# Kernel optimization log

Hardware: AMD Instinct MI355X
Metric: run time of the kernel (lower is better)

The kernel has to match this reference:

```python
import jax, jax.numpy as jnp
import numpy as np

HIDDEN = 512
HEADS = 8
HEAD_DIM = HIDDEN // HEADS


def setup_inputs() -> dict:
    key = jax.random.key(0)
    ks = jax.random.split(key, 12)
    B, N, C = 4, 2048, HIDDEN
    s = 1.0 / np.sqrt(C)
    inp = {
        "query_content": jax.random.normal(ks[0], (B, N, C), dtype=jnp.float32),
        "query_pos": jax.random.uniform(ks[1], (B, N, 4), dtype=jnp.float32),
        "Wq": jax.random.uniform(ks[2], (C, C), jnp.float32, -s, s),
        "bq": jax.random.uniform(ks[3], (C,), jnp.float32, -s, s),
        "Wk": jax.random.uniform(ks[4], (C, C), jnp.float32, -s, s),
        "bk": jax.random.uniform(ks[5], (C,), jnp.float32, -s, s),
        "Wv": jax.random.uniform(ks[6], (C, C), jnp.float32, -s, s),
        "bv": jax.random.uniform(ks[7], (C,), jnp.float32, -s, s),
        "Wo": jax.random.uniform(ks[8], (C, C), jnp.float32, -s, s),
        "bo": jax.random.uniform(ks[9], (C,), jnp.float32, -s, s),
        "gamma": jnp.ones((C,), jnp.float32),
        "beta": jnp.zeros((C,), jnp.float32),
    }
    return inp


def _iof_bias(query_pos):
    # query_pos: [B, N, 4] -> bias [B, N, N] = -0.1 * sqrt(dx^2 + dy^2 + eps)
    x = query_pos[..., 0]
    y = query_pos[..., 1]
    dx = jnp.abs(x[:, :, None] - x[:, None, :])
    dy = jnp.abs(y[:, :, None] - y[:, None, :])
    dist = jnp.sqrt(dx * dx + dy * dy + 1e-8)
    return -0.1 * dist


def reference(query_content, query_pos, Wq, bq, Wk, bk, Wv, bv, Wo, bo, gamma, beta):
    B, N, C = query_content.shape
    H, D = HEADS, HEAD_DIM
    # torch Linear: x @ W.T + b
    Q = (query_content @ Wq.T + bq).reshape(B, N, H, D).transpose(0, 2, 1, 3)
    K = (query_content @ Wk.T + bk).reshape(B, N, H, D).transpose(0, 2, 1, 3)
    V = (query_content @ Wv.T + bv).reshape(B, N, H, D).transpose(0, 2, 1, 3)
    scores = jnp.einsum("bhnd,bhmd->bhnm", Q, K) / jnp.sqrt(jnp.float32(D))
    scores = scores + _iof_bias(query_pos)[:, None, :, :]
    attn = jax.nn.softmax(scores, axis=-1)
    out = jnp.einsum("bhnm,bhmd->bhnd", attn, V)
    out = out.transpose(0, 2, 1, 3).reshape(B, N, C)
    out = out @ Wo.T + bo
    h = out + query_content
    mu = jnp.mean(h, axis=-1, keepdims=True)
    var = jnp.var(h, axis=-1, keepdims=True)
    return (h - mu) / jnp.sqrt(var + 1e-5) * gamma + beta
```

## Files before the change

kernel.cpp:

```cpp
#include <hip/hip_runtime.h>
#include <hip/hip_bf16.h>

#define C_DIM 512
#define H_NUM 8
#define D_DIM 64
#define B_NUM 4
#define N_SEQ 2048
#define M_TOT (B_NUM*N_SEQ)

typedef unsigned short u16;
typedef unsigned int   u32;
typedef __attribute__((ext_vector_type(8))) short short8;
typedef __attribute__((ext_vector_type(4))) float f32x4;

#define MFMA16 __builtin_amdgcn_mfma_f32_16x16x32_bf16

__device__ __forceinline__ u16 f2b(float f) {
    union { float f; u32 u; } v; v.f = f;
    u32 r = v.u + 0x7FFFu + ((v.u >> 16) & 1u);
    return (u16)(r >> 16);
}
__device__ __forceinline__ float fexp2(float x) {
    float r;
    asm("v_exp_f32 %0, %1" : "=v"(r) : "v"(x));
    return r;
}
__device__ __forceinline__ float b2f_lo(u32 u) {
    union { u32 u; float f; } v; v.u = u << 16; return v.f;
}
__device__ __forceinline__ float b2f_hi(u32 u) {
    union { u32 u; float f; } v; v.u = u & 0xFFFF0000u; return v.f;
}
__device__ __forceinline__ void gload16(const u16* g, u16* l) {
    __builtin_amdgcn_global_load_lds(
        (const __attribute__((address_space(1))) void*)g,
        (__attribute__((address_space(3))) void*)l, 16, 0, 0);
}
__device__ __forceinline__ void cast8(const float* s, u16* d) {
    const float4* p = (const float4*)s;
    float4 a = p[0], b = p[1];
    short8 v;
    v[0] = (short)f2b(a.x); v[1] = (short)f2b(a.y);
    v[2] = (short)f2b(a.z); v[3] = (short)f2b(a.w);
    v[4] = (short)f2b(b.x); v[5] = (short)f2b(b.y);
    v[6] = (short)f2b(b.z); v[7] = (short)f2b(b.w);
    *(short8*)d = v;
}

__global__ __launch_bounds__(256) void k_prep(const float* __restrict__ qc,
                                              const float* __restrict__ Wq,
                                              const float* __restrict__ Wk,
                                              const float* __restrict__ Wv,
                                              const float* __restrict__ Wo,
                                              const float* __restrict__ bq,
                                              const float* __restrict__ bk,
                                              const float* __restrict__ bv,
                                              const float* __restrict__ bo,
                                              const float* __restrict__ qpos,
                                              u16* __restrict__ xb,
                                              u16* __restrict__ wb,
                                              float* __restrict__ bqkv,
                                              u16* __restrict__ bias)
{
    const int bid = blockIdx.x, t = threadIdx.x;
    if (bid < 2048) {
        int i = bid * 256 + t;
        cast8(qc + (size_t)i * 8, xb + (size_t)i * 8);
    } else if (bid < 2560) {
        int r = bid - 2048;
        int y = r >> 7;
        const float* s = (y == 0) ? Wq : (y == 1) ? Wk : (y == 2) ? Wv : Wo;
        int i = (r & 127) * 256 + t;
        cast8(s + (size_t)i * 8, wb + (size_t)y * 262144 + (size_t)i * 8);
    } else if (bid < 2568) {
        int idx = (bid - 2560) * 256 + t;
        float v = idx < 512 ? bq[idx] : idx < 1024 ? bk[idx - 512]
                : idx < 1536 ? bv[idx - 1024] : bo[idx - 1536];
        bqkv[idx] = v;
    } else {
        int r = bid - 2568;
        int i = r & 2047, b = r >> 11;
        const float4 qi = *(const float4*)(qpos + (size_t)(b * 2048 + i) * 4);
        const float4* pj = (const float4*)(qpos + ((size_t)b * 2048 + t * 8) * 4);
        const float NC = -0.1f * 1.4426950408889634f;
        short8 v;
        #pragma unroll
        for (int jj = 0; jj < 8; ++jj) {
            float4 pk = pj[jj];
            float dx = qi.x - pk.x, dy = qi.y - pk.y;
            float d2 = fmaf(dx, dx, fmaf(dy, dy, 1e-8f));
            v[jj] = (short)f2b(sqrtf(d2) * NC);
        }
        *(short8*)(bias + (size_t)(b * 2048 + i) * 2048 + t * 8) = v;
    }
}

__global__ __launch_bounds__(256) void k_gemm(const u16* __restrict__ A,
                                              const u16* __restrict__ Bw,
                                              const float* __restrict__ bias,
                                              const float* __restrict__ qc,
                                              u16* __restrict__ oq,
                                              u16* __restrict__ ok,
                                              u16* __restrict__ ov,
                                              float* __restrict__ outf,
                                              int fixed_mode)
{
    __shared__ alignas(16) u16 la[3][4][128][8];
    __shared__ alignas(16) u16 lb[3][4][128][8];
    const int t = threadIdx.x;
    const int nwg = gridDim.x * gridDim.y;
    const int wgid = blockIdx.y * gridDim.x + blockIdx.x;
    const int swz = (wgid & 7) * (nwg >> 3) + (wgid >> 3);
    const int ntn = gridDim.y;
    const int m0 = (swz / ntn) * 128, n0 = (swz % ntn) * 128;
    const int w = t >> 6, l = t & 63, lr = l & 15, kg = l >> 4;
    const int wm = w >> 1, wn = w & 1;
    const int NS = C_DIM / 32;

    f32x4 acc[4][4] = {};

    const int srow = t & 127;
    const u16* As0 = A + (size_t)(m0 + srow) * C_DIM + (t >> 7) * 8;
    const u16* Bs0 = Bw + (size_t)(n0 + srow) * C_DIM + (t >> 7) * 8;

    #pragma unroll
    for (int s = 0; s < 2; ++s) {
        u16* ldA = (u16*)la[s] + w * 512;
        u16* ldB = (u16*)lb[s] + w * 512;
        gload16(As0 + s * 32,      ldA);
        gload16(As0 + s * 32 + 16, ldA + 2048);
        gload16(Bs0 + s * 32,      ldB);
        gload16(Bs0 + s * 32 + 16, ldB + 2048);
    }
    asm volatile("s_waitcnt vmcnt(4)" ::: "memory");
    __builtin_amdgcn_s_barrier();

    for (int s = 0; s < NS; ++s) {
        const int bi = s % 3;
        if (s + 2 < NS) {
            const int bn = (s + 2) % 3;
            u16* ldA = (u16*)la[bn] + w * 512;
            u16* ldB = (u16*)lb[bn] + w * 512;
            gload16(As0 + (s + 2) * 32,      ldA);
            gload16(As0 + (s + 2) * 32 + 16, ldA + 2048);
            gload16(Bs0 + (s + 2) * 32,      ldB);
            gload16(Bs0 + (s + 2) * 32 + 16, ldB + 2048);
        }
        __builtin_amdgcn_sched_barrier(0);

        short8 af[4], bf[4];
        #pragma unroll
        for (int fm = 0; fm < 4; ++fm)
            af[fm] = *(const short8*)la[bi][kg][wm * 64 + fm * 16 + lr];
        #pragma unroll
        for (int fn = 0; fn < 4; ++fn)
            bf[fn] = *(const short8*)lb[bi][kg][wn * 64 + fn * 16 + lr];
        __builtin_amdgcn_s_setprio(1);
        #pragma unroll
        for (int fm = 0; fm < 4; ++fm)
        #pragma unroll
        for (int fn = 0; fn < 4; ++fn)
            acc[fm][fn] = MFMA16(af[fm], bf[fn], acc[fm][fn], 0, 0, 0);
        __builtin_amdgcn_s_setprio(0);

        if (s + 1 < NS) {
            if (s + 2 < NS) asm volatile("s_waitcnt vmcnt(4)" ::: "memory");
            else            asm volatile("s_waitcnt vmcnt(0)" ::: "memory");
            __builtin_amdgcn_s_barrier();
        }
    }

    const int mode = (fixed_mode == 3) ? 3 : (n0 >> 9);

    if (mode == 3) {
        #pragma unroll
        for (int fm = 0; fm < 4; ++fm)
        #pragma unroll
        for (int fn = 0; fn < 4; ++fn) {
            int c = n0 + wn * 64 + fn * 16 + lr;
            float bv_ = bias[c];
            #pragma unroll
            for (int i = 0; i < 4; ++i) {
                int m = m0 + wm * 64 + fm * 16 + kg * 4 + i;
                outf[(size_t)m * C_DIM + c] = acc[fm][fn][i] + bv_ + qc[(size_t)m * C_DIM + c];
            }
        }
    } else if (mode == 2) {
        #pragma unroll
        for (int fm = 0; fm < 4; ++fm)
        #pragma unroll
        for (int fn = 0; fn < 4; ++fn) {
            int c = n0 + wn * 64 + fn * 16 + lr;
            int cc = c & 511, h = cc >> 6, d = cc & 63;
            float bv_ = bias[c];
            int m = m0 + wm * 64 + fm * 16 + kg * 4;
            int bb = m >> 11, n = m & 2047;
            uint2 pk;
            pk.x = ((u32)f2b(acc[fm][fn][1] + bv_) << 16) | f2b(acc[fm][fn][0] + bv_);
            pk.y = ((u32)f2b(acc[fm][fn][3] + bv_) << 16) | f2b(acc[fm][fn][2] + bv_);
            *(uint2*)(ov + ((size_t)(bb * H_NUM + h) * D_DIM + d) * N_SEQ + n) = pk;
        }
    } else {
        u16* outb = (mode == 0) ? oq : ok;
        #pragma unroll
        for (int fm = 0; fm < 4; ++fm)
        #pragma unroll
        for (int fn = 0; fn < 4; ++fn) {
            int c = n0 + wn * 64 + fn * 16 + lr;
            int cc = c & 511, h = cc >> 6, d = cc & 63;
            float bv_ = bias[c];
            #pragma unroll
            for (int i = 0; i < 4; ++i) {
                int m = m0 + wm * 64 + fm * 16 + kg * 4 + i;
                int bb = m >> 11, n = m & 2047;
                outb[((size_t)(bb * H_NUM + h) * N_SEQ + n) * D_DIM + d] = f2b(bv_ + acc[fm][fn][i]);
            }
        }
    }
}

__global__ __launch_bounds__(512, 4) void k_flash(const u16* __restrict__ Q,
                                                  const u16* __restrict__ K,
                                                  const u16* __restrict__ Vt,
                                                  const u16* __restrict__ bias,
                                                  u16* __restrict__ attn_out)
{
    __shared__ alignas(16) u16 kbuf[3][64][64];
    __shared__ alignas(16) u16 vbuf[3][64][64];
    __shared__ alignas(16) u16 pbuf[8][16][64];

    const int t = threadIdx.x;
    const int w = t >> 6, l = t & 63, lr = l & 15, g = l >> 4;
    const int flat = blockIdx.y * 16 + blockIdx.x;
    const int h = flat >> 6, b = (flat >> 4) & 3, qt = flat & 15;
    const int bh = b * H_NUM + h;
    const int q = qt * 128 + w * 16 + lr;
    const int sx = lr & 7;

    const float SC = 0.125f * 1.4426950408889634f;
    const int NT = N_SEQ / 64;

    const u16* Qb = Q + ((size_t)bh * N_SEQ + q) * D_DIM;
    const u16* Kb = K + (size_t)bh * N_SEQ * D_DIM;
    const u16* Vb = Vt + (size_t)bh * D_DIM * N_SEQ;
    const u16* Bb = bias + ((size_t)b * N_SEQ + q) * N_SEQ;

    short8 aq0 = *(const short8*)(Qb + g * 8);
    short8 aq1 = *(const short8*)(Qb + 32 + g * 8);

    const int sr = t >> 3;
    const int ssl = (t & 7) ^ (sr & 7);
    const u16* gK = Kb + (size_t)sr * D_DIM + ssl * 8;
    const u16* gV = Vb + (size_t)sr * N_SEQ + ssl * 8;

    f32x4 acc[4] = {};
    float lac0 = 0.f, lac1 = 0.f, lac2 = 0.f, lac3 = 0.f;
    uint2 bcur[4], bnxt[4];

    gload16(gK,              (u16*)&kbuf[0][0][0] + w * 512);
    gload16(gV,              (u16*)&vbuf[0][0][0] + w * 512);
    gload16(gK + 64 * D_DIM, (u16*)&kbuf[1][0][0] + w * 512);
    gload16(gV + 64,         (u16*)&vbuf[1][0][0] + w * 512);
    __builtin_amdgcn_sched_barrier(0);
    #pragma unroll
    for (int fn = 0; fn < 4; ++fn)
        bcur[fn] = *(const uint2*)(Bb + fn * 16 + g * 4);
    __builtin_amdgcn_sched_barrier(0);
    asm volatile("s_waitcnt vmcnt(6)" ::: "memory");
    __builtin_amdgcn_s_barrier();

    for (int kt = 0; kt < NT; ++kt) {
        const int bi = kt % 3;
        if (kt + 1 < NT) {
            #pragma unroll
            for (int fn = 0; fn < 4; ++fn)
                bnxt[fn] = *(const uint2*)(Bb + (kt + 1) * 64 + fn * 16 + g * 4);
        }
        __builtin_amdgcn_sched_barrier(0);
        if (kt + 2 < NT) {
            const int bn = (kt + 2) % 3;
            gload16(gK + (size_t)(kt + 2) * 64 * D_DIM, (u16*)&kbuf[bn][0][0] + w * 512);
            gload16(gV + (kt + 2) * 64,                 (u16*)&vbuf[bn][0][0] + w * 512);
        }
        __builtin_amdgcn_sched_barrier(0);

        f32x4 st[4] = {};
        __builtin_amdgcn_s_setprio(1);
        #pragma unroll
        for (int fn = 0; fn < 4; ++fn) {
            short8 ak0 = *(const short8*)&kbuf[bi][fn * 16 + lr][(g ^ sx) * 8];
            short8 ak1 = *(const short8*)&kbuf[bi][fn * 16 + lr][((4 + g) ^ sx) * 8];
            st[fn] = MFMA16(ak0, aq0, st[fn], 0, 0, 0);
            st[fn] = MFMA16(ak1, aq1, st[fn], 0, 0, 0);
        }
        __builtin_amdgcn_s_setprio(0);

        float sv[16];
        #pragma unroll
        for (int fn = 0; fn < 4; ++fn) {
            sv[fn * 4 + 0] = fmaf(st[fn][0], SC, b2f_lo(bcur[fn].x));
            sv[fn * 4 + 1] = fmaf(st[fn][1], SC, b2f_hi(bcur[fn].x));
            sv[fn * 4 + 2] = fmaf(st[fn][2], SC, b2f_lo(bcur[fn].y));
            sv[fn * 4 + 3] = fmaf(st[fn][3], SC, b2f_hi(bcur[fn].y));
        }
        #pragma unroll
        for (int j = 0; j < 4; ++j)  { sv[j]  = fexp2(sv[j]);  lac0 += sv[j]; }
        #pragma unroll
        for (int j = 4; j < 8; ++j)  { sv[j]  = fexp2(sv[j]);  lac1 += sv[j]; }
        #pragma unroll
        for (int j = 8; j < 12; ++j) { sv[j]  = fexp2(sv[j]);  lac2 += sv[j]; }
        #pragma unroll
        for (int j = 12; j < 16; ++j){ sv[j]  = fexp2(sv[j]);  lac3 += sv[j]; }

        #pragma unroll
        for (int fn = 0; fn < 4; ++fn) {
            union { float f; u32 u; } p0, p1, p2, p3;
            p0.f = sv[fn * 4 + 0]; p1.f = sv[fn * 4 + 1];
            p2.f = sv[fn * 4 + 2]; p3.f = sv[fn * 4 + 3];
            uint2 pk;
            pk.x = (p1.u & 0xFFFF0000u) | (p0.u >> 16);
            pk.y = (p3.u & 0xFFFF0000u) | (p2.u >> 16);
            int slot = fn * 2 + (g >> 1);
            *(uint2*)&pbuf[w][lr][(slot ^ sx) * 8 + (g & 1) * 4] = pk;
        }
        asm volatile("s_waitcnt lgkmcnt(0)" ::: "memory");
        __builtin_amdgcn_sched_barrier(0);

        short8 bp0 = *(const short8*)&pbuf[w][lr][(g ^ sx) * 8];
        short8 bp1 = *(const short8*)&pbuf[w][lr][((4 + g) ^ sx) * 8];

        __builtin_amdgcn_s_setprio(1);
        #pragma unroll
        for (int df = 0; df < 4; ++df) {
            short8 av0 = *(const short8*)&vbuf[bi][df * 16 + lr][(g ^ sx) * 8];
            short8 av1 = *(const short8*)&vbuf[bi][df * 16 + lr][((4 + g) ^ sx) * 8];
            acc[df] = MFMA16(av0, bp0, acc[df], 0, 0, 0);
            acc[df] = MFMA16(av1, bp1, acc[df], 0, 0, 0);
        }
        __builtin_amdgcn_s_setprio(0);

        #pragma unroll
        for (int fn = 0; fn < 4; ++fn) bcur[fn] = bnxt[fn];

        if (kt + 1 < NT) {
            if (kt + 2 < NT) asm volatile("s_waitcnt vmcnt(6)" ::: "memory");
            else             asm volatile("s_waitcnt vmcnt(4)" ::: "memory");
            __builtin_amdgcn_s_barrier();
        }
    }

    float l_run = (lac0 + lac1) + (lac2 + lac3);
    l_run += __shfl_xor(l_run, 16);
    l_run += __shfl_xor(l_run, 32);
    float rl;
    asm("v_rcp_f32 %0, %1" : "=v"(rl) : "v"(l_run));
    rl = rl * (2.f - l_run * rl);
    u16* ob = attn_out + ((size_t)(b * N_SEQ + q)) * C_DIM + h * D_DIM + g * 4;
    #pragma unroll
    for (int df = 0; df < 4; ++df) {
        u32 w0 = ((u32)f2b(acc[df][1] * rl) << 16) | f2b(acc[df][0] * rl);
        u32 w1 = ((u32)f2b(acc[df][3] * rl) << 16) | f2b(acc[df][2] * rl);
        uint2 pk; pk.x = w0; pk.y = w1;
        *(uint2*)(ob + df * 16) = pk;
    }
}

__global__ __launch_bounds__(256) void k_ln(const float* __restrict__ hbuf,
                                            const float* __restrict__ gamma,
                                            const float* __restrict__ beta,
                                            float* __restrict__ out)
{
    const int r = blockIdx.x;
    const int t = threadIdx.x;
    const size_t base = (size_t)r * C_DIM;
    float2 h01 = *(const float2*)(hbuf + base + t * 2);
    float s = h01.x + h01.y, sq = h01.x * h01.x + h01.y * h01.y;
    #pragma unroll
    for (int m = 1; m < 64; m <<= 1) {
        s += __shfl_xor(s, m);
        sq += __shfl_xor(sq, m);
    }
    __shared__ float ss[4], ssq[4];
    int w = t >> 6;
    if ((t & 63) == 0) { ss[w] = s; ssq[w] = sq; }
    __syncthreads();
    s = ss[0] + ss[1] + ss[2] + ss[3];
    sq = ssq[0] + ssq[1] + ssq[2] + ssq[3];
    float mu = s * (1.f / C_DIM);
    float var = sq * (1.f / C_DIM) - mu * mu;
    float inv = rsqrtf(var + 1e-5f);
    float2 g01 = *(const float2*)(gamma + t * 2);
    float2 b01 = *(const float2*)(beta + t * 2);
    float2 o;
    o.x = (h01.x - mu) * inv * g01.x + b01.x;
    o.y = (h01.y - mu) * inv * g01.y + b01.y;
    *(float2*)(out + base + t * 2) = o;
}

extern "C" void kernel_launch(void* const* d_in, const int* in_sizes, int n_in,
                              void* d_out, int out_size, void* d_ws, size_t ws_size,
                              hipStream_t stream)
{
    const float* qc    = (const float*)d_in[0];
    const float* qpos  = (const float*)d_in[1];
    const float* Wq    = (const float*)d_in[2];
    const float* bq    = (const float*)d_in[3];
    const float* Wk    = (const float*)d_in[4];
    const float* bk    = (const float*)d_in[5];
    const float* Wv    = (const float*)d_in[6];
    const float* bv    = (const float*)d_in[7];
    const float* Wo    = (const float*)d_in[8];
    const float* bo    = (const float*)d_in[9];
    const float* gamma = (const float*)d_in[10];
    const float* beta  = (const float*)d_in[11];
    float* out = (float*)d_out;

    char* ws = (char*)d_ws;
    const size_t MB = 1024 * 1024;
    u16*   bias_ws = (u16*)(ws);
    u16*   xb_ws   = (u16*)(ws + 32 * MB);
    u16*   wb_ws   = (u16*)(ws + 40 * MB);
    float* bqkv_ws = (float*)(ws + 42 * MB);
    u16*   q_ws    = (u16*)(ws + 43 * MB);
    u16*   k_ws    = (u16*)(ws + 51 * MB);
    u16*   v_ws    = (u16*)(ws + 59 * MB);
    u16*   a_ws    = (u16*)(ws + 75 * MB);
    float* p_ws    = (float*)(ws + 43 * MB);

    k_prep<<<dim3(10760), 256, 0, stream>>>(qc, Wq, Wk, Wv, Wo, bq, bk, bv, bo,
                                            qpos, xb_ws, wb_ws, bqkv_ws, bias_ws);
    k_gemm<<<dim3(M_TOT / 128, 12), 256, 0, stream>>>(xb_ws, wb_ws, bqkv_ws, nullptr,
                                                      q_ws, k_ws, v_ws, nullptr, -1);
    k_flash<<<dim3(16, 32), 512, 0, stream>>>(q_ws, k_ws, v_ws, bias_ws, a_ws);
    k_gemm<<<dim3(M_TOT / 128, 4), 256, 0, stream>>>(a_ws, wb_ws + 1536 * 512,
                                                     bqkv_ws + 1536, qc,
                                                     nullptr, nullptr, nullptr, p_ws, 3);
    k_ln<<<dim3(M_TOT), 256, 0, stream>>>(p_ws, gamma, beta, out);
}
```

Baseline: 170.3 us.

## Switch flash attention to 32x32 MFMA with 4 waves of 32 queries each

Rewrites the attention kernel to use 32x32x16 bf16 MFMA instead of 16x16x32: each wave now owns 32 query rows and the block shrinks from 512 to 256 threads, still covering 128 queries. K/V staging, bias loads, P-buffer layout and output write are remapped to the 32x32 register layout. The larger MFMA tile gives each wave more reuse per LDS read, at the cost of more accumulator registers and fewer waves per block to hide latency.

```diff
diff --git a/kernel.cpp b/kernel.cpp
--- a/kernel.cpp
+++ b/kernel.cpp
@@ -12,8 +12,10 @@
 typedef unsigned int   u32;
 typedef __attribute__((ext_vector_type(8))) short short8;
 typedef __attribute__((ext_vector_type(4))) float f32x4;
+typedef __attribute__((ext_vector_type(16))) float f32x16;
 
 #define MFMA16 __builtin_amdgcn_mfma_f32_16x16x32_bf16
+#define MFMA32 __builtin_amdgcn_mfma_f32_32x32x16_bf16
 
 __device__ __forceinline__ u16 f2b(float f) {
     union { float f; u32 u; } v; v.f = f;
@@ -219,7 +221,7 @@
     }
 }
 
-__global__ __launch_bounds__(512, 4) void k_flash(const u16* __restrict__ Q,
+__global__ __launch_bounds__(256, 2) void k_flash(const u16* __restrict__ Q,
                                                   const u16* __restrict__ K,
                                                   const u16* __restrict__ Vt,
                                                   const u16* __restrict__ bias,
@@ -227,15 +229,15 @@
 {
     __shared__ alignas(16) u16 kbuf[3][64][64];
     __shared__ alignas(16) u16 vbuf[3][64][64];
-    __shared__ alignas(16) u16 pbuf[8][16][64];
+    __shared__ alignas(16) u16 pbuf[4][32][64];
 
     const int t = threadIdx.x;
-    const int w = t >> 6, l = t & 63, lr = l & 15, g = l >> 4;
+    const int w = t >> 6, l = t & 63;
+    const int qc_ = l & 31, hi = l >> 5, sx = l & 7;
     const int flat = blockIdx.y * 16 + blockIdx.x;
     const int h = flat >> 6, b = (flat >> 4) & 3, qt = flat & 15;
     const int bh = b * H_NUM + h;
-    const int q = qt * 128 + w * 16 + lr;
-    const int sx = lr & 7;
+    const int q = qt * 128 + w * 32 + qc_;
 
     const float SC = 0.125f * 1.4426950408889634f;
     const int NT = N_SEQ / 64;
@@ -245,123 +247,140 @@
     const u16* Vb = Vt + (size_t)bh * D_DIM * N_SEQ;
     const u16* Bb = bias + ((size_t)b * N_SEQ + q) * N_SEQ;
 
-    short8 aq0 = *(const short8*)(Qb + g * 8);
-    short8 aq1 = *(const short8*)(Qb + 32 + g * 8);
+    short8 aq[4];
+    #pragma unroll
+    for (int s = 0; s < 4; ++s)
+        aq[s] = *(const short8*)(Qb + s * 16 + hi * 8);
 
     const int sr = t >> 3;
     const int ssl = (t & 7) ^ (sr & 7);
     const u16* gK = Kb + (size_t)sr * D_DIM + ssl * 8;
     const u16* gV = Vb + (size_t)sr * N_SEQ + ssl * 8;
 
-    f32x4 acc[4] = {};
+    f32x16 acc0 = {}, acc1 = {};
     float lac0 = 0.f, lac1 = 0.f, lac2 = 0.f, lac3 = 0.f;
-    uint2 bcur[4], bnxt[4];
-
-    gload16(gK,              (u16*)&kbuf[0][0][0] + w * 512);
-    gload16(gV,              (u16*)&vbuf[0][0][0] + w * 512);
-    gload16(gK + 64 * D_DIM, (u16*)&kbuf[1][0][0] + w * 512);
-    gload16(gV + 64,         (u16*)&vbuf[1][0][0] + w * 512);
+    uint2 bcur[8], bnxt[8];
+
+#define STAGE(bn, kto) { \
+    u16* kd = (u16*)&kbuf[bn][0][0] + w * 512; \
+    u16* vd = (u16*)&vbuf[bn][0][0] + w * 512; \
+    const u16* k1 = gK + (size_t)(kto) * 64 * D_DIM; \
+    const u16* v1 = gV + (kto) * 64; \
+    gload16(k1, kd);  gload16(k1 + 32 * D_DIM, kd + 2048); \
+    gload16(v1, vd);  gload16(v1 + (size_t)32 * N_SEQ, vd + 2048); }
+
+    STAGE(0, 0);
     __builtin_amdgcn_sched_barrier(0);
     #pragma unroll
-    for (int fn = 0; fn < 4; ++fn)
-        bcur[fn] = *(const uint2*)(Bb + fn * 16 + g * 4);
+    for (int u = 0; u < 8; ++u) {
+        int mblk = u >> 2, rg = u & 3;
+        bcur[u] = *(const uint2*)(Bb + 32 * mblk + 8 * rg + 4 * hi);
+    }
     __builtin_amdgcn_sched_barrier(0);
-    asm volatile("s_waitcnt vmcnt(6)" ::: "memory");
+    STAGE(1, 1);
+    __builtin_amdgcn_sched_barrier(0);
+    asm volatile("s_waitcnt vmcnt(12)" ::: "memory");
     __builtin_amdgcn_s_barrier();
 
     for (int kt = 0; kt < NT; ++kt) {
         const int bi = kt % 3;
         if (kt + 1 < NT) {
             #pragma unroll
-            for (int fn = 0; fn < 4; ++fn)
-                bnxt[fn] = *(const uint2*)(Bb + (kt + 1) * 64 + fn * 16 + g * 4);
+            for (int u = 0; u < 8; ++u) {
+                int mblk = u >> 2, rg = u & 3;
+                bnxt[u] = *(const uint2*)(Bb + (kt + 1) * 64 + 32 * mblk + 8 * rg + 4 * hi);
+            }
         }
         __builtin_amdgcn_sched_barrier(0);
         if (kt + 2 < NT) {
             const int bn = (kt + 2) % 3;
-            gload16(gK + (size_t)(kt + 2) * 64 * D_DIM, (u16*)&kbuf[bn][0][0] + w * 512);
-            gload16(gV + (kt + 2) * 64,                 (u16*)&vbuf[bn][0][0] + w * 512);
+            STAGE(bn, kt + 2);
         }
         __builtin_amdgcn_sched_barrier(0);
 
-        f32x4 st[4] = {};
+        f32x16 st0 = {}, st1 = {};
         __builtin_amdgcn_s_setprio(1);
         #pragma unroll
-        for (int fn = 0; fn < 4; ++fn) {
-            short8 ak0 = *(const short8*)&kbuf[bi][fn * 16 + lr][(g ^ sx) * 8];
-            short8 ak1 = *(const short8*)&kbuf[bi][fn * 16 + lr][((4 + g) ^ sx) * 8];
-            st[fn] = MFMA16(ak0, aq0, st[fn], 0, 0, 0);
-            st[fn] = MFMA16(ak1, aq1, st[fn], 0, 0, 0);
+        for (int s = 0; s < 4; ++s) {
+            short8 ak0 = *(const short8*)&kbuf[bi][qc_][((2 * s + hi) ^ sx) * 8];
+            short8 ak1 = *(const short8*)&kbuf[bi][32 + qc_][((2 * s + hi) ^ sx) * 8];
+            st0 = MFMA32(ak0, aq[s], st0, 0, 0, 0);
+            st1 = MFMA32(ak1, aq[s], st1, 0, 0, 0);
         }
         __builtin_amdgcn_s_setprio(0);
 
-        float sv[16];
-        #pragma unroll
-        for (int fn = 0; fn < 4; ++fn) {
-            sv[fn * 4 + 0] = fmaf(st[fn][0], SC, b2f_lo(bcur[fn].x));
-            sv[fn * 4 + 1] = fmaf(st[fn][1], SC, b2f_hi(bcur[fn].x));
-            sv[fn * 4 + 2] = fmaf(st[fn][2], SC, b2f_lo(bcur[fn].y));
-            sv[fn * 4 + 3] = fmaf(st[fn][3], SC, b2f_hi(bcur[fn].y));
-        }
-        #pragma unroll
-        for (int j = 0; j < 4; ++j)  { sv[j]  = fexp2(sv[j]);  lac0 += sv[j]; }
-        #pragma unroll
-        for (int j = 4; j < 8; ++j)  { sv[j]  = fexp2(sv[j]);  lac1 += sv[j]; }
-        #pragma unroll
-        for (int j = 8; j < 12; ++j) { sv[j]  = fexp2(sv[j]);  lac2 += sv[j]; }
-        #pragma unroll
-        for (int j = 12; j < 16; ++j){ sv[j]  = fexp2(sv[j]);  lac3 += sv[j]; }
-
-        #pragma unroll
-        for (int fn = 0; fn < 4; ++fn) {
+        #pragma unroll
+        for (int rg = 0; rg < 4; ++rg) {
+            float s0 = fmaf(st0[4 * rg + 0], SC, b2f_lo(bcur[rg].x));
+            float s1 = fmaf(st0[4 * rg + 1], SC, b2f_hi(bcur[rg].x));
+            float s2 = fmaf(st0[4 * rg + 2], SC, b2f_lo(bcur[rg].y));
+            float s3 = fmaf(st0[4 * rg + 3], SC, b2f_hi(bcur[rg].y));
+            s0 = fexp2(s0); s1 = fexp2(s1); s2 = fexp2(s2); s3 = fexp2(s3);
+            lac0 += s0 + s1; lac1 += s2 + s3;
             union { float f; u32 u; } p0, p1, p2, p3;
-            p0.f = sv[fn * 4 + 0]; p1.f = sv[fn * 4 + 1];
-            p2.f = sv[fn * 4 + 2]; p3.f = sv[fn * 4 + 3];
+            p0.f = s0; p1.f = s1; p2.f = s2; p3.f = s3;
             uint2 pk;
             pk.x = (p1.u & 0xFFFF0000u) | (p0.u >> 16);
             pk.y = (p3.u & 0xFFFF0000u) | (p2.u >> 16);
-            int slot = fn * 2 + (g >> 1);
-            *(uint2*)&pbuf[w][lr][(slot ^ sx) * 8 + (g & 1) * 4] = pk;
+            *(uint2*)((u16*)&pbuf[w][qc_][0] + ((rg ^ sx) * 8 + hi * 4)) = pk;
+        }
+        #pragma unroll
+        for (int rg = 0; rg < 4; ++rg) {
+            float s0 = fmaf(st1[4 * rg + 0], SC, b2f_lo(bcur[4 + rg].x));
+            float s1 = fmaf(st1[4 * rg + 1], SC, b2f_hi(bcur[4 + rg].x));
+            float s2 = fmaf(st1[4 * rg + 2], SC, b2f_lo(bcur[4 + rg].y));
+            float s3 = fmaf(st1[4 * rg + 3], SC, b2f_hi(bcur[4 + rg].y));
+            s0 = fexp2(s0); s1 = fexp2(s1); s2 = fexp2(s2); s3 = fexp2(s3);
+            lac2 += s0 + s1; lac3 += s2 + s3;
+            union { float f; u32 u; } p0, p1, p2, p3;
+            p0.f = s0; p1.f = s1; p2.f = s2; p3.f = s3;
+            uint2 pk;
+            pk.x = (p1.u & 0xFFFF0000u) | (p0.u >> 16);
+            pk.y = (p3.u & 0xFFFF0000u) | (p2.u >> 16);
+            *(uint2*)((u16*)&pbuf[w][qc_][0] + (((4 + rg) ^ sx) * 8 + hi * 4)) = pk;
         }
         asm volatile("s_waitcnt lgkmcnt(0)" ::: "memory");
         __builtin_amdgcn_sched_barrier(0);
 
-        short8 bp0 = *(const short8*)&pbuf[w][lr][(g ^ sx) * 8];
-        short8 bp1 = *(const short8*)&pbuf[w][lr][((4 + g) ^ sx) * 8];
-
         __builtin_amdgcn_s_setprio(1);
         #pragma unroll
-        for (int df = 0; df < 4; ++df) {
-            short8 av0 = *(const short8*)&vbuf[bi][df * 16 + lr][(g ^ sx) * 8];
-            short8 av1 = *(const short8*)&vbuf[bi][df * 16 + lr][((4 + g) ^ sx) * 8];
-            acc[df] = MFMA16(av0, bp0, acc[df], 0, 0, 0);
-            acc[df] = MFMA16(av1, bp1, acc[df], 0, 0, 0);
+        for (int s = 0; s < 4; ++s) {
+            short8 bp  = *(const short8*)((u16*)&pbuf[w][qc_][0] + (((2 * s + hi) ^ sx) * 8));
+            short8 av0 = *(const short8*)&vbuf[bi][qc_][((2 * s + hi) ^ sx) * 8];
+            short8 av1 = *(const short8*)&vbuf[bi][32 + qc_][((2 * s + hi) ^ sx) * 8];
+            acc0 = MFMA32(av0, bp, acc0, 0, 0, 0);
+            acc1 = MFMA32(av1, bp, acc1, 0, 0, 0);
         }
         __builtin_amdgcn_s_setprio(0);
 
         #pragma unroll
-        for (int fn = 0; fn < 4; ++fn) bcur[fn] = bnxt[fn];
+        for (int u = 0; u < 8; ++u) bcur[u] = bnxt[u];
 
         if (kt + 1 < NT) {
-            if (kt + 2 < NT) asm volatile("s_waitcnt vmcnt(6)" ::: "memory");
-            else             asm volatile("s_waitcnt vmcnt(4)" ::: "memory");
+            if (kt + 2 < NT) asm volatile("s_waitcnt vmcnt(12)" ::: "memory");
+            else             asm volatile("s_waitcnt vmcnt(8)" ::: "memory");
             __builtin_amdgcn_s_barrier();
         }
     }
+#undef STAGE
 
     float l_run = (lac0 + lac1) + (lac2 + lac3);
-    l_run += __shfl_xor(l_run, 16);
     l_run += __shfl_xor(l_run, 32);
     float rl;
     asm("v_rcp_f32 %0, %1" : "=v"(rl) : "v"(l_run));
     rl = rl * (2.f - l_run * rl);
-    u16* ob = attn_out + ((size_t)(b * N_SEQ + q)) * C_DIM + h * D_DIM + g * 4;
+    u16* ob = attn_out + ((size_t)(b * N_SEQ + q)) * C_DIM + h * D_DIM;
     #pragma unroll
-    for (int df = 0; df < 4; ++df) {
-        u32 w0 = ((u32)f2b(acc[df][1] * rl) << 16) | f2b(acc[df][0] * rl);
-        u32 w1 = ((u32)f2b(acc[df][3] * rl) << 16) | f2b(acc[df][2] * rl);
-        uint2 pk; pk.x = w0; pk.y = w1;
-        *(uint2*)(ob + df * 16) = pk;
+    for (int rg = 0; rg < 4; ++rg) {
+        int d0 = 8 * rg + 4 * hi;
+        uint2 pk;
+        pk.x = ((u32)f2b(acc0[4 * rg + 1] * rl) << 16) | f2b(acc0[4 * rg + 0] * rl);
+        pk.y = ((u32)f2b(acc0[4 * rg + 3] * rl) << 16) | f2b(acc0[4 * rg + 2] * rl);
+        *(uint2*)(ob + d0) = pk;
+        uint2 pk2;
+        pk2.x = ((u32)f2b(acc1[4 * rg + 1] * rl) << 16) | f2b(acc1[4 * rg + 0] * rl);
+        pk2.y = ((u32)f2b(acc1[4 * rg + 3] * rl) << 16) | f2b(acc1[4 * rg + 2] * rl);
+        *(uint2*)(ob + 32 + d0) = pk2;
     }
 }
 
@@ -431,7 +450,7 @@
                                             qpos, xb_ws, wb_ws, bqkv_ws, bias_ws);
     k_gemm<<<dim3(M_TOT / 128, 12), 256, 0, stream>>>(xb_ws, wb_ws, bqkv_ws, nullptr,
                                                       q_ws, k_ws, v_ws, nullptr, -1);
-    k_flash<<<dim3(16, 32), 512, 0, stream>>>(q_ws, k_ws, v_ws, bias_ws, a_ws);
+    k_flash<<<dim3(16, 32), 256, 0, stream>>>(q_ws, k_ws, v_ws, bias_ws, a_ws);
     k_gemm<<<dim3(M_TOT / 128, 4), 256, 0, stream>>>(a_ws, wb_ws + 1536 * 512,
                                                      bqkv_ws + 1536, qc,
                                                      nullptr, nullptr, nullptr, p_ws, 3);
```

Measured after the change: 174.7 us. 2.6% more time.
